# Kernel optimization log

Hardware: AMD Instinct MI355X
Metric: run time of the kernel (lower is better)

The kernel has to match this reference:

```python
import jax, jax.numpy as jnp
import numpy as np

N = 50000       # nodes
E = 1600000     # edges (avg degree 32)
D = 128         # in = hidden = out channels
H = 4           # attention heads


def setup_inputs() -> dict:
    key = jax.random.key(0)
    ks = jax.random.split(key, 9)
    s = 1.0 / np.sqrt(D)  # ~kaiming-scale linear weights
    return {
        "x": jax.random.normal(ks[0], (N, D), jnp.float32),
        "Wk": jax.random.normal(ks[1], (D, D), jnp.float32) * s,
        "bk": jnp.zeros((D,), jnp.float32),
        "Wq": jax.random.normal(ks[2], (D, D), jnp.float32) * s,
        "bq": jnp.zeros((D,), jnp.float32),
        "Wv": jax.random.normal(ks[3], (D, D), jnp.float32) * s,
        "bv": jnp.zeros((D,), jnp.float32),
        "src": jax.random.randint(ks[4], (E,), 0, N, dtype=jnp.int32),
        "dst": jax.random.randint(ks[5], (E,), 0, N, dtype=jnp.int32),
    }


def reference(x, Wk, bk, Wq, bq, Wv, bv, src, dst):
    n = x.shape[0]
    heads = H
    dk = Wk.shape[0] // heads
    dv = Wv.shape[0] // heads
    # Dense projections (near-roofline GEMMs)
    k = (x @ Wk.T + bk).reshape(n, heads, dk)
    q = (x @ Wq.T + bq).reshape(n, heads, dk)
    v = (x @ Wv.T + bv).reshape(n, heads, dv)
    # u_dot_v: per-edge per-head dot product (NO 1/sqrt(dk) scaling in source)
    scores = jnp.einsum('ehd,ehd->eh', k[src], q[dst])  # [E,H]
    # edge_softmax: softmax over incoming edges of each destination node
    m = jax.ops.segment_max(scores, dst, num_segments=n)        # [N,H]
    p = jnp.exp(scores - m[dst])                                 # [E,H]
    denom = jax.ops.segment_sum(p, dst, num_segments=n)         # [N,H]
    alpha = p / denom[dst]                                       # [E,H]
    # u_mul_e + sum: weighted scatter-aggregation of source values
    res = jax.ops.segment_sum(v[src] * alpha[:, :, None], dst, num_segments=n)  # [N,H,dv]
    # original: view(batch_size, -1, out_channels) with batch_size = N -> [N,1,out]
    return res.reshape(n, 1, heads * dv)
```

## Files before the change

kernel.cpp:

```cpp
#include <hip/hip_runtime.h>
#include <hip/hip_bf16.h>
#include <hip/hip_fp16.h>

#define NN 50000
#define NE 1600000
#define DD 128
#define HH 4
#define BSH2 5
#define NBKT2 1563
#define NBP2 2048
#define CAP 1408
#define PCHUNK 8192
#define NPB 196
#define GEMMB 782
#define MIDB (GEMMB + NPB)

typedef __attribute__((ext_vector_type(8))) short short8;
typedef __attribute__((ext_vector_type(4))) float floatx4;
typedef __attribute__((ext_vector_type(2))) _Float16 h2;

__device__ inline h2 as_h2(unsigned u) {
    union { unsigned u; h2 h; } c; c.u = u; return c.h;
}

__device__ inline float dot4(h2 a01, h2 a23, h2 b01, h2 b23) {
#if defined(__has_builtin) && __has_builtin(__builtin_amdgcn_fdot2)
    return __builtin_amdgcn_fdot2(a01, b01, __builtin_amdgcn_fdot2(a23, b23, 0.f, false), false);
#else
    return (float)a01.x * (float)b01.x + (float)a01.y * (float)b01.y +
           (float)a23.x * (float)b23.x + (float)a23.y * (float)b23.y;
#endif
}

__global__ __launch_bounds__(256) void prep_w(
    const float* __restrict__ Wk, const float* __restrict__ Wq, const float* __restrict__ Wv,
    unsigned short* __restrict__ hi, unsigned short* __restrict__ lo, int* __restrict__ bcur)
{
    int j = blockIdx.x * 256 + threadIdx.x;
    if (j < NBP2) bcur[j] = 0;
    if (j >= 3 * DD * DD) return;
    int which = j / (DD * DD);
    int off = j - which * (DD * DD);
    const float* W = (which == 0) ? Wk : (which == 1) ? Wq : Wv;
    float w = W[off];
    unsigned int b = __float_as_uint(w);
    unsigned short h = (unsigned short)(b >> 16);
    float hf = __uint_as_float((unsigned int)h << 16);
    float l = w - hf;
    hi[j] = h;
    lo[j] = (unsigned short)(__float_as_uint(l) >> 16);
}

__global__ __launch_bounds__(256) void mid(
    const float* __restrict__ x,
    const unsigned short* __restrict__ whi, const unsigned short* __restrict__ wlo,
    const float* __restrict__ bk, const float* __restrict__ bq, const float* __restrict__ bv,
    uint4* __restrict__ kvpack, __half* __restrict__ qh,
    const int* __restrict__ src, const int* __restrict__ dst,
    int* __restrict__ bcur, int* __restrict__ epack)
{
    __shared__ __align__(16) unsigned char smem[32768];

    if (blockIdx.x < GEMMB) {
        unsigned short (*stage)[4096] = (unsigned short (*)[4096])smem;
        int wave = threadIdx.x >> 6;
        int tile = blockIdx.x * 4 + wave;
        int n0 = tile * 16;
        if (n0 >= NN) return;
        int lane = threadIdx.x & 63;
        int m    = lane & 15;
        int quad = lane >> 4;

        const float* xrow = x + (size_t)(n0 + m) * DD + quad * 8;
        short8 ah[4], al[4];
#pragma unroll
        for (int ks = 0; ks < 4; ++ks) {
            const float* xr = xrow + ks * 32;
            float4 t0 = *(const float4*)xr;
            float4 t1 = *(const float4*)(xr + 4);
            float xv[8] = {t0.x, t0.y, t0.z, t0.w, t1.x, t1.y, t1.z, t1.w};
#pragma unroll
            for (int j = 0; j < 8; ++j) {
                unsigned int b = __float_as_uint(xv[j]);
                unsigned short h = (unsigned short)(b >> 16);
                float hf = __uint_as_float((unsigned int)h << 16);
                float l = xv[j] - hf;
                ah[ks][j] = (short)h;
                al[ks][j] = (short)(__float_as_uint(l) >> 16);
            }
        }

        floatx4 acc[3][8];
#pragma unroll
        for (int p = 0; p < 3; ++p)
#pragma unroll
            for (int ct = 0; ct < 8; ++ct)
                acc[p][ct] = (floatx4){0.f, 0.f, 0.f, 0.f};

#pragma unroll
        for (int ks = 0; ks < 4; ++ks) {
#pragma unroll
            for (int p = 0; p < 3; ++p) {
                size_t base = (size_t)p * DD * DD + (size_t)m * DD + ks * 32 + quad * 8;
#pragma unroll
                for (int ct = 0; ct < 8; ++ct) {
                    size_t o = base + (size_t)ct * 16 * DD;
                    short8 bh = *(const short8*)(whi + o);
                    short8 bl = *(const short8*)(wlo + o);
                    acc[p][ct] = __builtin_amdgcn_mfma_f32_16x16x32_bf16(ah[ks], bh, acc[p][ct], 0, 0, 0);
                    acc[p][ct] = __builtin_amdgcn_mfma_f32_16x16x32_bf16(ah[ks], bl, acc[p][ct], 0, 0, 0);
                    acc[p][ct] = __builtin_amdgcn_mfma_f32_16x16x32_bf16(al[ks], bh, acc[p][ct], 0, 0, 0);
                }
            }
        }

        int col = lane & 15;
        unsigned short* st = stage[wave];
        uint4* st4 = (uint4*)st;

#pragma unroll
        for (int ct = 0; ct < 8; ++ct) {
            int j = ct * 16 + col;
            int g = j >> 2, slot = j & 3;
            float biask = bk[j], biasv = bv[j];
#pragma unroll
            for (int r = 0; r < 4; ++r) {
                int row = quad * 4 + r;
                st[row * 256 + g * 8 + slot]     = __half_as_ushort(__float2half(acc[0][ct][r] + biask));
                st[row * 256 + g * 8 + 4 + slot] = __half_as_ushort(__float2half(acc[2][ct][r] + biasv));
            }
        }
#pragma unroll
        for (int t = 0; t < 8; ++t) {
            int flat = t * 64 + lane;
            kvpack[((size_t)n0 + (flat >> 5)) * 32 + (flat & 31)] = st4[flat];
        }

#pragma unroll
        for (int ct = 0; ct < 8; ++ct) {
            int j = ct * 16 + col;
            float biasq = bq[j];
#pragma unroll
            for (int r = 0; r < 4; ++r) {
                int row = quad * 4 + r;
                st[row * 128 + j] = __half_as_ushort(__float2half(acc[1][ct][r] + biasq));
            }
        }
#pragma unroll
        for (int t = 0; t < 4; ++t) {
            int flat = t * 64 + lane;
            ((uint4*)qh)[((size_t)n0 + (flat >> 4)) * 16 + (flat & 15)] = st4[flat];
        }
    } else {
        int* h  = (int*)smem;
        int* c2 = h + NBP2;
        int pb = blockIdx.x - GEMMB;
        int b0 = pb * PCHUNK;
        int n = min(PCHUNK, NE - b0);
        for (int i = threadIdx.x; i < NBP2; i += 256) h[i] = 0;
        __syncthreads();
        for (int i = threadIdx.x; i < n; i += 256)
            atomicAdd(&h[dst[b0 + i] >> BSH2], 1);
        __syncthreads();
        for (int i = threadIdx.x; i < NBP2; i += 256)
            c2[i] = h[i] ? i * CAP + atomicAdd(&bcur[i], h[i]) : 0;
        __syncthreads();
        for (int i = threadIdx.x; i < n; i += 256) {
            int d = dst[b0 + i];
            int s = src[b0 + i];
            int bkt = d >> BSH2;
            int pos = atomicAdd(&c2[bkt], 1);
            if (pos < (bkt + 1) * CAP)
                epack[pos] = ((d & 31) << 16) | s;
        }
    }
}

__global__ __launch_bounds__(256) void gat_bucket(
    const __half* __restrict__ qh, const uint4* __restrict__ kvpack,
    const int* __restrict__ epack, const int* __restrict__ bcur,
    float* __restrict__ out)
{
    __shared__ int hist[32];
    __shared__ int cur[32];
    __shared__ int begs[33];
    __shared__ unsigned short els[CAP];
    int b = blockIdx.x;
    int cnt = min(bcur[b], CAP);
    int base = b * CAP;
    int n0 = b << BSH2;
    int nnodes = min(32, NN - n0);
    int tid = threadIdx.x;

    if (tid < 32) hist[tid] = 0;
    __syncthreads();
    for (int e = tid; e < cnt; e += 256)
        atomicAdd(&hist[epack[base + e] >> 16], 1);
    __syncthreads();
    if (tid < 32) {
        int c = hist[tid], inc = c;
#pragma unroll
        for (int d = 1; d < 32; d <<= 1) {
            int t = __shfl_up(inc, d);
            if (tid >= d) inc += t;
        }
        int excl = inc - c;
        begs[tid] = excl;
        cur[tid]  = excl;
        if (tid == 31) begs[32] = excl + c;
    }
    __syncthreads();
    for (int e = tid; e < cnt; e += 256) {
        int p = epack[base + e];
        int pos = atomicAdd(&cur[p >> 16], 1);
        els[pos] = (unsigned short)(p & 0xFFFF);
    }
    __syncthreads();

    int il = tid & 31;
    int hw = tid >> 5;

    for (int nl = hw; nl < nnodes; nl += 8) {
        int node = n0 + nl;
        int beg = begs[nl], end = begs[nl + 1];

        uint2 qq = *(const uint2*)(qh + (size_t)node * 128 + il * 4);
        h2 qh01 = as_h2(qq.x), qh23 = as_h2(qq.y);

        float m = -INFINITY, ssum = 0.f;
        float o0 = 0.f, o1 = 0.f, o2 = 0.f, o3 = 0.f;

        for (int j = beg; j < end; j += 8) {
            int nh = min(8, end - j);
            uint4 kvv[8];
#pragma unroll
            for (int i = 0; i < 8; ++i) {
                int s = els[j + ((i < nh) ? i : 0)];
                kvv[i] = kvpack[(size_t)s * 32 + il];
            }
            float p[8];
#pragma unroll
            for (int i = 0; i < 8; ++i) {
                float t = dot4(as_h2(kvv[i].x), as_h2(kvv[i].y), qh01, qh23);
                t += __shfl_xor(t, 1);
                t += __shfl_xor(t, 2);
                t += __shfl_xor(t, 4);
                p[i] = (i < nh) ? t : -INFINITY;
            }
            float gm = fmaxf(fmaxf(fmaxf(p[0], p[1]), fmaxf(p[2], p[3])),
                             fmaxf(fmaxf(p[4], p[5]), fmaxf(p[6], p[7])));
            float nm = fmaxf(m, gm);
            float nmc = fmaxf(nm, -1e30f);
            float scale = __expf(m - nmc);
            ssum *= scale; o0 *= scale; o1 *= scale; o2 *= scale; o3 *= scale;
#pragma unroll
            for (int i = 0; i < 8; ++i) {
                float w = __expf(p[i] - nmc);
                ssum += w;
                o0 += w * (float)as_h2(kvv[i].z).x;
                o1 += w * (float)as_h2(kvv[i].z).y;
                o2 += w * (float)as_h2(kvv[i].w).x;
                o3 += w * (float)as_h2(kvv[i].w).y;
            }
            m = nm;
        }

        float invd = (ssum > 0.f) ? 1.f / ssum : 0.f;
        float4 r = {o0 * invd, o1 * invd, o2 * invd, o3 * invd};
        *(float4*)(out + (size_t)node * DD + il * 4) = r;
    }
}

extern "C" void kernel_launch(void* const* d_in, const int* in_sizes, int n_in,
                              void* d_out, int out_size, void* d_ws, size_t ws_size,
                              hipStream_t stream) {
    const float* x  = (const float*)d_in[0];
    const float* Wk = (const float*)d_in[1];
    const float* bk = (const float*)d_in[2];
    const float* Wq = (const float*)d_in[3];
    const float* bq = (const float*)d_in[4];
    const float* Wv = (const float*)d_in[5];
    const float* bv = (const float*)d_in[6];
    const int* src = (const int*)d_in[7];
    const int* dst = (const int*)d_in[8];

    uint4*  kvpack = (uint4*)d_ws;
    __half* qh     = (__half*)(kvpack + (size_t)NN * 32);
    unsigned short* whi = (unsigned short*)(qh + (size_t)NN * DD);
    unsigned short* wlo = whi + (size_t)3 * DD * DD;
    int* epack = (int*)(wlo + (size_t)3 * DD * DD);
    int* bcur  = epack + (size_t)NBKT2 * CAP;

    prep_w<<<(3 * DD * DD + 255) / 256, 256, 0, stream>>>(Wk, Wq, Wv, whi, wlo, bcur);
    mid<<<MIDB, 256, 0, stream>>>(x, whi, wlo, bk, bq, bv, kvpack, qh, src, dst, bcur, epack);
    gat_bucket<<<NBKT2, 256, 0, stream>>>(qh, kvpack, epack, bcur, (float*)d_out);
}
```

Before: 306.0 us.

## Replace global atomic bucketing with histogram-scan-scatter and prefetch KV gathers

Edge bucketing by destination is split into three phases: per-chunk histograms written to global memory, a column-wise exclusive scan over chunks per bin, and a separate scatter kernel that uses the precomputed offsets. This drops the global atomicAdd on bucket counters and makes edge placement within each bucket deterministic, at the cost of two extra kernel launches and a histogram round trip through global memory. Separately, the aggregation loop software-pipelines the KV gathers, loading the next group of 8 neighbors while computing the current one, which raises register pressure.

```diff
diff --git a/kernel.cpp b/kernel.cpp
--- a/kernel.cpp
+++ b/kernel.cpp
@@ -34,10 +34,9 @@
 
 __global__ __launch_bounds__(256) void prep_w(
     const float* __restrict__ Wk, const float* __restrict__ Wq, const float* __restrict__ Wv,
-    unsigned short* __restrict__ hi, unsigned short* __restrict__ lo, int* __restrict__ bcur)
+    unsigned short* __restrict__ hi, unsigned short* __restrict__ lo)
 {
     int j = blockIdx.x * 256 + threadIdx.x;
-    if (j < NBP2) bcur[j] = 0;
     if (j >= 3 * DD * DD) return;
     int which = j / (DD * DD);
     int off = j - which * (DD * DD);
@@ -56,8 +55,7 @@
     const unsigned short* __restrict__ whi, const unsigned short* __restrict__ wlo,
     const float* __restrict__ bk, const float* __restrict__ bq, const float* __restrict__ bv,
     uint4* __restrict__ kvpack, __half* __restrict__ qh,
-    const int* __restrict__ src, const int* __restrict__ dst,
-    int* __restrict__ bcur, int* __restrict__ epack)
+    const int* __restrict__ dst, int* __restrict__ histg)
 {
     __shared__ __align__(16) unsigned char smem[32768];
 
@@ -152,8 +150,7 @@
             ((uint4*)qh)[((size_t)n0 + (flat >> 4)) * 16 + (flat & 15)] = st4[flat];
         }
     } else {
-        int* h  = (int*)smem;
-        int* c2 = h + NBP2;
+        int* h = (int*)smem;
         int pb = blockIdx.x - GEMMB;
         int b0 = pb * PCHUNK;
         int n = min(PCHUNK, NE - b0);
@@ -163,16 +160,48 @@
             atomicAdd(&h[dst[b0 + i] >> BSH2], 1);
         __syncthreads();
         for (int i = threadIdx.x; i < NBP2; i += 256)
-            c2[i] = h[i] ? i * CAP + atomicAdd(&bcur[i], h[i]) : 0;
-        __syncthreads();
-        for (int i = threadIdx.x; i < n; i += 256) {
-            int d = dst[b0 + i];
-            int s = src[b0 + i];
-            int bkt = d >> BSH2;
-            int pos = atomicAdd(&c2[bkt], 1);
-            if (pos < (bkt + 1) * CAP)
-                epack[pos] = ((d & 31) << 16) | s;
-        }
+            histg[(size_t)pb * NBP2 + i] = h[i];
+    }
+}
+
+__global__ __launch_bounds__(64) void scan_bins(int* __restrict__ histg, int* __restrict__ bcur)
+{
+    int b = blockIdx.x * 64 + threadIdx.x;
+    if (b >= NBP2) return;
+    int run = 0;
+    int c = 0;
+    int t[16];
+    for (; c + 16 <= NPB; c += 16) {
+#pragma unroll
+        for (int u = 0; u < 16; ++u) t[u] = histg[(size_t)(c + u) * NBP2 + b];
+#pragma unroll
+        for (int u = 0; u < 16; ++u) { histg[(size_t)(c + u) * NBP2 + b] = run; run += t[u]; }
+    }
+    for (; c < NPB; ++c) {
+        int tt = histg[(size_t)c * NBP2 + b];
+        histg[(size_t)c * NBP2 + b] = run; run += tt;
+    }
+    bcur[b] = run;
+}
+
+__global__ __launch_bounds__(256) void scatter_part(
+    const int* __restrict__ src, const int* __restrict__ dst,
+    const int* __restrict__ histg, int* __restrict__ epack)
+{
+    __shared__ int c2[NBP2];
+    int pb = blockIdx.x;
+    int b0 = pb * PCHUNK;
+    int n = min(PCHUNK, NE - b0);
+    for (int i = threadIdx.x; i < NBP2; i += 256)
+        c2[i] = i * CAP + histg[(size_t)pb * NBP2 + i];
+    __syncthreads();
+    for (int i = threadIdx.x; i < n; i += 256) {
+        int d = dst[b0 + i];
+        int s = src[b0 + i];
+        int bkt = d >> BSH2;
+        int pos = atomicAdd(&c2[bkt], 1);
+        if (pos < (bkt + 1) * CAP)
+            epack[pos] = ((d & 31) << 16) | s;
     }
 }
 
@@ -219,6 +248,7 @@
 
     int il = tid & 31;
     int hw = tid >> 5;
+    const uint4* kvb = kvpack + il;
 
     for (int nl = hw; nl < nnodes; nl += 8) {
         int node = n0 + nl;
@@ -230,13 +260,27 @@
         float m = -INFINITY, ssum = 0.f;
         float o0 = 0.f, o1 = 0.f, o2 = 0.f, o3 = 0.f;
 
+        uint4 kvv[8];
+        int nh = end - beg; if (nh > 8) nh = 8;
+        if (nh > 0) {
+#pragma unroll
+            for (int i = 0; i < 8; ++i) {
+                int s = els[beg + ((i < nh) ? i : 0)];
+                kvv[i] = kvb[(size_t)s * 32];
+            }
+        }
+
         for (int j = beg; j < end; j += 8) {
-            int nh = min(8, end - j);
-            uint4 kvv[8];
-#pragma unroll
-            for (int i = 0; i < 8; ++i) {
-                int s = els[j + ((i < nh) ? i : 0)];
-                kvv[i] = kvpack[(size_t)s * 32 + il];
+            int jn = j + 8;
+            int rem = end - jn;
+            uint4 kvn[8];
+            if (rem > 0) {
+                int nhc = (rem > 8) ? 8 : rem;
+#pragma unroll
+                for (int i = 0; i < 8; ++i) {
+                    int s = els[jn + ((i < nhc) ? i : 0)];
+                    kvn[i] = kvb[(size_t)s * 32];
+                }
             }
             float p[8];
 #pragma unroll
@@ -263,6 +307,9 @@
                 o3 += w * (float)as_h2(kvv[i].w).y;
             }
             m = nm;
+#pragma unroll
+            for (int i = 0; i < 8; ++i) kvv[i] = kvn[i];
+            nh = (rem > 8) ? 8 : rem;
         }
 
         float invd = (ssum > 0.f) ? 1.f / ssum : 0.f;
@@ -290,8 +337,11 @@
     unsigned short* wlo = whi + (size_t)3 * DD * DD;
     int* epack = (int*)(wlo + (size_t)3 * DD * DD);
     int* bcur  = epack + (size_t)NBKT2 * CAP;
-
-    prep_w<<<(3 * DD * DD + 255) / 256, 256, 0, stream>>>(Wk, Wq, Wv, whi, wlo, bcur);
-    mid<<<MIDB, 256, 0, stream>>>(x, whi, wlo, bk, bq, bv, kvpack, qh, src, dst, bcur, epack);
+    int* histg = bcur + NBP2;
+
+    prep_w<<<(3 * DD * DD + 255) / 256, 256, 0, stream>>>(Wk, Wq, Wv, whi, wlo);
+    mid<<<MIDB, 256, 0, stream>>>(x, whi, wlo, bk, bq, bv, kvpack, qh, dst, histg);
+    scan_bins<<<32, 64, 0, stream>>>(histg, bcur);
+    scatter_part<<<NPB, 256, 0, stream>>>(src, dst, histg, epack);
     gat_bucket<<<NBKT2, 256, 0, stream>>>(qh, kvpack, epack, bcur, (float*)d_out);
 }
```

New measurement: 355.2 us. 1.16x slower.

## Stage weight hi-parts in LDS with persistent GEMM blocks and prefetch KV gathers

Applied to the files above, without the earlier changes.

The projection GEMM becomes persistent: 560 blocks loop over node tiles one projection at a time. Each block loads the bf16-high weight half into swizzled LDS once per projection and reuses it across tiles, instead of re-reading both weight halves from global memory for every tile. Projections now run sequentially per block, which re-reads x three times and writes K and V as separate interleaved 8-byte stores. The aggregation kernel also double-buffers the per-edge KV gathers, loading the next 8 neighbours before computing the current batch, at the cost of more registers.

```diff
diff --git a/kernel.cpp b/kernel.cpp
--- a/kernel.cpp
+++ b/kernel.cpp
@@ -12,8 +12,8 @@
 #define CAP 1408
 #define PCHUNK 8192
 #define NPB 196
-#define GEMMB 782
-#define MIDB (GEMMB + NPB)
+#define NGB 560
+#define MIDB (NGB + NPB)
 
 typedef __attribute__((ext_vector_type(8))) short short8;
 typedef __attribute__((ext_vector_type(4))) float floatx4;
@@ -55,106 +55,102 @@
     const float* __restrict__ x,
     const unsigned short* __restrict__ whi, const unsigned short* __restrict__ wlo,
     const float* __restrict__ bk, const float* __restrict__ bq, const float* __restrict__ bv,
-    uint4* __restrict__ kvpack, __half* __restrict__ qh,
+    uint2* __restrict__ kv2, uint4* __restrict__ qh4,
     const int* __restrict__ src, const int* __restrict__ dst,
     int* __restrict__ bcur, int* __restrict__ epack)
 {
-    __shared__ __align__(16) unsigned char smem[32768];
-
-    if (blockIdx.x < GEMMB) {
-        unsigned short (*stage)[4096] = (unsigned short (*)[4096])smem;
-        int wave = threadIdx.x >> 6;
-        int tile = blockIdx.x * 4 + wave;
-        int n0 = tile * 16;
-        if (n0 >= NN) return;
-        int lane = threadIdx.x & 63;
-        int m    = lane & 15;
-        int quad = lane >> 4;
-
-        const float* xrow = x + (size_t)(n0 + m) * DD + quad * 8;
-        short8 ah[4], al[4];
-#pragma unroll
-        for (int ks = 0; ks < 4; ++ks) {
-            const float* xr = xrow + ks * 32;
-            float4 t0 = *(const float4*)xr;
-            float4 t1 = *(const float4*)(xr + 4);
-            float xv[8] = {t0.x, t0.y, t0.z, t0.w, t1.x, t1.y, t1.z, t1.w};
-#pragma unroll
-            for (int j = 0; j < 8; ++j) {
-                unsigned int b = __float_as_uint(xv[j]);
-                unsigned short h = (unsigned short)(b >> 16);
-                float hf = __uint_as_float((unsigned int)h << 16);
-                float l = xv[j] - hf;
-                ah[ks][j] = (short)h;
-                al[ks][j] = (short)(__float_as_uint(l) >> 16);
-            }
-        }
-
-        floatx4 acc[3][8];
-#pragma unroll
-        for (int p = 0; p < 3; ++p)
-#pragma unroll
-            for (int ct = 0; ct < 8; ++ct)
-                acc[p][ct] = (floatx4){0.f, 0.f, 0.f, 0.f};
-
-#pragma unroll
-        for (int ks = 0; ks < 4; ++ks) {
-#pragma unroll
-            for (int p = 0; p < 3; ++p) {
-                size_t base = (size_t)p * DD * DD + (size_t)m * DD + ks * 32 + quad * 8;
+    __shared__ __align__(16) unsigned char smem[49152];
+
+    if (blockIdx.x < NGB) {
+        uint4* wl4 = (uint4*)smem;
+        int tid = threadIdx.x;
+        int wave = tid >> 6, lane = tid & 63;
+        int m = lane & 15, quad = lane >> 4;
+        unsigned short* st = (unsigned short*)(smem + 32768 + wave * 4096);
+        uint4* st4 = (uint4*)st;
+        uint2* st2 = (uint2*)st;
+
+        for (int pp = 0; pp < 3; ++pp) {
+            int wm = (pp == 0) ? 0 : (pp == 1) ? 2 : 1;
+            const uint4* gh = (const uint4*)whi + (size_t)wm * 2048;
+            __syncthreads();
+            for (int g = tid; g < 2048; g += 256) {
+                int l = (g & ~15) | ((g ^ (g >> 4)) & 15);
+                wl4[l] = gh[g];
+            }
+            __syncthreads();
+            const unsigned short* wloP = wlo + (size_t)wm * (DD * DD);
+            const float* bias = (pp == 0) ? bk : (pp == 1) ? bv : bq;
+            float bs[8];
+#pragma unroll
+            for (int ct = 0; ct < 8; ++ct) bs[ct] = bias[ct * 16 + m];
+
+            for (int tile = blockIdx.x * 4 + wave; tile < 3125; tile += NGB * 4) {
+                int n0 = tile * 16;
+                const float* xrow = x + (size_t)(n0 + m) * DD + quad * 8;
+                short8 ah[4], al[4];
+#pragma unroll
+                for (int ks = 0; ks < 4; ++ks) {
+                    const float* xr = xrow + ks * 32;
+                    float4 t0 = *(const float4*)xr;
+                    float4 t1 = *(const float4*)(xr + 4);
+                    float xv[8] = {t0.x, t0.y, t0.z, t0.w, t1.x, t1.y, t1.z, t1.w};
+#pragma unroll
+                    for (int j = 0; j < 8; ++j) {
+                        unsigned int b = __float_as_uint(xv[j]);
+                        unsigned short h = (unsigned short)(b >> 16);
+                        float hf = __uint_as_float((unsigned int)h << 16);
+                        float l = xv[j] - hf;
+                        ah[ks][j] = (short)h;
+                        al[ks][j] = (short)(__float_as_uint(l) >> 16);
+                    }
+                }
+
+                floatx4 acc[8];
+#pragma unroll
+                for (int ct = 0; ct < 8; ++ct) acc[ct] = (floatx4){0.f, 0.f, 0.f, 0.f};
+
+#pragma unroll
+                for (int ks = 0; ks < 4; ++ks) {
+#pragma unroll
+                    for (int ct = 0; ct < 8; ++ct) {
+                        int r = ct * 16 + m;
+                        short8 bh = ((const short8*)wl4)[r * 16 + ((ks * 4 + quad) ^ m)];
+                        short8 bl = *(const short8*)(wloP + (size_t)r * 128 + ks * 32 + quad * 8);
+                        acc[ct] = __builtin_amdgcn_mfma_f32_16x16x32_bf16(ah[ks], bh, acc[ct], 0, 0, 0);
+                        acc[ct] = __builtin_amdgcn_mfma_f32_16x16x32_bf16(ah[ks], bl, acc[ct], 0, 0, 0);
+                        acc[ct] = __builtin_amdgcn_mfma_f32_16x16x32_bf16(al[ks], bh, acc[ct], 0, 0, 0);
+                    }
+                }
+
 #pragma unroll
                 for (int ct = 0; ct < 8; ++ct) {
-                    size_t o = base + (size_t)ct * 16 * DD;
-                    short8 bh = *(const short8*)(whi + o);
-                    short8 bl = *(const short8*)(wlo + o);
-                    acc[p][ct] = __builtin_amdgcn_mfma_f32_16x16x32_bf16(ah[ks], bh, acc[p][ct], 0, 0, 0);
-                    acc[p][ct] = __builtin_amdgcn_mfma_f32_16x16x32_bf16(ah[ks], bl, acc[p][ct], 0, 0, 0);
-                    acc[p][ct] = __builtin_amdgcn_mfma_f32_16x16x32_bf16(al[ks], bh, acc[p][ct], 0, 0, 0);
-                }
-            }
-        }
-
-        int col = lane & 15;
-        unsigned short* st = stage[wave];
-        uint4* st4 = (uint4*)st;
-
-#pragma unroll
-        for (int ct = 0; ct < 8; ++ct) {
-            int j = ct * 16 + col;
-            int g = j >> 2, slot = j & 3;
-            float biask = bk[j], biasv = bv[j];
-#pragma unroll
-            for (int r = 0; r < 4; ++r) {
-                int row = quad * 4 + r;
-                st[row * 256 + g * 8 + slot]     = __half_as_ushort(__float2half(acc[0][ct][r] + biask));
-                st[row * 256 + g * 8 + 4 + slot] = __half_as_ushort(__float2half(acc[2][ct][r] + biasv));
-            }
-        }
-#pragma unroll
-        for (int t = 0; t < 8; ++t) {
-            int flat = t * 64 + lane;
-            kvpack[((size_t)n0 + (flat >> 5)) * 32 + (flat & 31)] = st4[flat];
-        }
-
-#pragma unroll
-        for (int ct = 0; ct < 8; ++ct) {
-            int j = ct * 16 + col;
-            float biasq = bq[j];
-#pragma unroll
-            for (int r = 0; r < 4; ++r) {
-                int row = quad * 4 + r;
-                st[row * 128 + j] = __half_as_ushort(__float2half(acc[1][ct][r] + biasq));
-            }
-        }
-#pragma unroll
-        for (int t = 0; t < 4; ++t) {
-            int flat = t * 64 + lane;
-            ((uint4*)qh)[((size_t)n0 + (flat >> 4)) * 16 + (flat & 15)] = st4[flat];
+                    int j = ct * 16 + m;
+#pragma unroll
+                    for (int r = 0; r < 4; ++r)
+                        st[(quad * 4 + r) * 128 + j] = __half_as_ushort(__float2half(acc[ct][r] + bs[ct]));
+                }
+                if (pp < 2) {
+                    int voff = (pp == 1) ? 1 : 0;
+#pragma unroll
+                    for (int t = 0; t < 8; ++t) {
+                        int flat = t * 64 + lane;
+                        int row = flat >> 5, gg = flat & 31;
+                        kv2[((size_t)(n0 + row)) * 64 + gg * 2 + voff] = st2[flat];
+                    }
+                } else {
+#pragma unroll
+                    for (int t = 0; t < 4; ++t) {
+                        int flat = t * 64 + lane;
+                        qh4[((size_t)(n0 + (flat >> 4))) * 16 + (flat & 15)] = st4[flat];
+                    }
+                }
+            }
         }
     } else {
         int* h  = (int*)smem;
         int* c2 = h + NBP2;
-        int pb = blockIdx.x - GEMMB;
+        int pb = blockIdx.x - NGB;
         int b0 = pb * PCHUNK;
         int n = min(PCHUNK, NE - b0);
         for (int i = threadIdx.x; i < NBP2; i += 256) h[i] = 0;
@@ -219,6 +215,7 @@
 
     int il = tid & 31;
     int hw = tid >> 5;
+    const uint4* kvb = kvpack + il;
 
     for (int nl = hw; nl < nnodes; nl += 8) {
         int node = n0 + nl;
@@ -230,13 +227,27 @@
         float m = -INFINITY, ssum = 0.f;
         float o0 = 0.f, o1 = 0.f, o2 = 0.f, o3 = 0.f;
 
+        uint4 kvv[8];
+        int nh = end - beg; if (nh > 8) nh = 8;
+        if (nh > 0) {
+#pragma unroll
+            for (int i = 0; i < 8; ++i) {
+                int s = els[beg + ((i < nh) ? i : 0)];
+                kvv[i] = kvb[(size_t)s * 32];
+            }
+        }
+
         for (int j = beg; j < end; j += 8) {
-            int nh = min(8, end - j);
-            uint4 kvv[8];
-#pragma unroll
-            for (int i = 0; i < 8; ++i) {
-                int s = els[j + ((i < nh) ? i : 0)];
-                kvv[i] = kvpack[(size_t)s * 32 + il];
+            int jn = j + 8;
+            int rem = end - jn;
+            uint4 kvn[8];
+            if (rem > 0) {
+                int nhc = (rem > 8) ? 8 : rem;
+#pragma unroll
+                for (int i = 0; i < 8; ++i) {
+                    int s = els[jn + ((i < nhc) ? i : 0)];
+                    kvn[i] = kvb[(size_t)s * 32];
+                }
             }
             float p[8];
 #pragma unroll
@@ -263,6 +274,9 @@
                 o3 += w * (float)as_h2(kvv[i].w).y;
             }
             m = nm;
+#pragma unroll
+            for (int i = 0; i < 8; ++i) kvv[i] = kvn[i];
+            nh = (rem > 8) ? 8 : rem;
         }
 
         float invd = (ssum > 0.f) ? 1.f / ssum : 0.f;
@@ -292,6 +306,7 @@
     int* bcur  = epack + (size_t)NBKT2 * CAP;
 
     prep_w<<<(3 * DD * DD + 255) / 256, 256, 0, stream>>>(Wk, Wq, Wv, whi, wlo, bcur);
-    mid<<<MIDB, 256, 0, stream>>>(x, whi, wlo, bk, bq, bv, kvpack, qh, src, dst, bcur, epack);
+    mid<<<MIDB, 256, 0, stream>>>(x, whi, wlo, bk, bq, bv, (uint2*)kvpack, (uint4*)qh,
+                                  src, dst, bcur, epack);
     gat_bucket<<<NBKT2, 256, 0, stream>>>(qh, kvpack, epack, bcur, (float*)d_out);
 }
```

Measured after the change: 291.3 us. 4.8% less time.
